# Kernel tuning notes

Measured on AMD Instinct MI355X. Metric: run time of the kernel, lower is better.

The kernel has to match this reference:

```python
import jax, jax.numpy as jnp
import numpy as np

B, S, D, H = 4, 2048, 512, 8
E = D // H  # d_head = 64

def setup_inputs() -> dict:
    key = jax.random.key(0)
    ks = jax.random.split(key, 10)
    s_in = (1.0 / np.sqrt(D))
    x  = jax.random.normal(ks[0], (B, S, D), dtype=jnp.float32)
    Wq = jax.random.normal(ks[1], (H, D, E), dtype=jnp.float32) * s_in
    bq = jax.random.normal(ks[2], (H, E), dtype=jnp.float32) * 0.01
    Wk = jax.random.normal(ks[3], (H, D, E), dtype=jnp.float32) * s_in
    bk = jax.random.normal(ks[4], (H, E), dtype=jnp.float32) * 0.01
    Wv = jax.random.normal(ks[5], (H, D, E), dtype=jnp.float32) * s_in
    bv = jax.random.normal(ks[6], (H, E), dtype=jnp.float32) * 0.01
    Wo = jax.random.normal(ks[7], (D, D), dtype=jnp.float32) * s_in
    bo = jax.random.normal(ks[8], (D,), dtype=jnp.float32) * 0.01
    return {"x": x, "Wq": Wq, "bq": bq, "Wk": Wk, "bk": bk,
            "Wv": Wv, "bv": bv, "Wo": Wo, "bo": bo}

def reference(x, Wq, bq, Wk, bk, Wv, bv, Wo, bo):
    B_, S_, D_ = x.shape
    # per-head projections (batched over head axis h)
    q = jnp.einsum('bsd,hde->bhse', x, Wq) + bq[None, :, None, :]
    k = jnp.einsum('bsd,hde->bhse', x, Wk) + bk[None, :, None, :]
    v = jnp.einsum('bsd,hde->bhse', x, Wv) + bv[None, :, None, :]
    # NOTE: original scales by d_model**-0.5 (full D), not d_head**-0.5
    scale = jnp.asarray(D_, x.dtype) ** -0.5
    scores = jnp.einsum('bhse,bhte->bhst', q, k) * scale  # [B,H,S,S]
    causal = jnp.tril(jnp.ones((S_, S_), dtype=bool))
    scores = jnp.where(causal[None, None], scores, -jnp.inf)
    attn = jax.nn.softmax(scores, axis=-1)
    out = jnp.einsum('bhst,bhte->bhse', attn, v)  # [B,H,S,E]
    # concat heads along feature dim (head-major), matching torch.cat
    out = out.transpose(0, 2, 1, 3).reshape(B_, S_, D_)
    return out @ Wo + bo  # final projection; dropout never applied in source
```

## Files before the change

### kernel.cpp

```cpp
#include <hip/hip_runtime.h>

typedef unsigned short u16;
typedef __bf16 bf16x8 __attribute__((ext_vector_type(8)));
typedef short s16x4 __attribute__((ext_vector_type(4)));
typedef short s16x8 __attribute__((ext_vector_type(8)));
typedef float f32x4 __attribute__((ext_vector_type(4)));

#define BB 4
#define SS 2048
#define DD 512
#define HH 8
#define EE 64
#define MM 8192
#define BHSE (BB*HH*SS*EE)

#define GLOBAL_AS __attribute__((address_space(1)))
#define LDS_AS    __attribute__((address_space(3)))

__device__ __forceinline__ float b2f(u16 u) {
    return __uint_as_float(((unsigned int)u) << 16);
}
__device__ __forceinline__ u16 f2b(float f) {
    unsigned int v = __float_as_uint(f);
    v += 0x7fffu + ((v >> 16) & 1u);
    return (u16)(v >> 16);
}
__device__ __forceinline__ float loadE(const void* p, size_t idx, int isbf16) {
    return isbf16 ? b2f(((const u16*)p)[idx]) : ((const float*)p)[idx];
}
__device__ __forceinline__ void load_lds16(const u16* g, u16* l) {
    __builtin_amdgcn_global_load_lds((GLOBAL_AS void*)g, (LDS_AS void*)l, 16, 0, 0);
}

__device__ __forceinline__ int detect_bf16_wave(const u16* x) {
    const int lane = threadIdx.x & 63;
    float a0 = fabsf(b2f(x[2 * lane]));
    float a1 = fabsf(b2f(x[2 * (lane + 64)]));
    int c0 = (a0 == 0.f) || (a0 > 1e-4f && a0 < 100.f);
    int c1 = (a1 == 0.f) || (a1 > 1e-4f && a1 < 100.f);
    int cnt = __popcll(__ballot(c0)) + __popcll(__ballot(c1));
    return cnt >= 96;
}

__global__ __launch_bounds__(256) void prep(
    const void* __restrict__ X,
    const void* __restrict__ Wq, const void* __restrict__ Wk,
    const void* __restrict__ Wv, const void* __restrict__ Wo,
    u16* __restrict__ Xb, u16* __restrict__ WT, u16* __restrict__ WoT,
    int* __restrict__ flag)
{
    const int isbf16 = detect_bf16_wave((const u16*)X);
    const int bid = blockIdx.x;
    const int tid = threadIdx.x;
    if (bid < 1024) {
        if (bid == 0 && tid == 0) *flag = isbf16;
        const size_t i0 = ((size_t)bid * 256 + tid) * 16;
        if (isbf16) {
            const uint4* src = (const uint4*)(((const u16*)X) + i0);
            uint4* dst = (uint4*)(Xb + i0);
            dst[0] = src[0];
            dst[1] = src[1];
        } else {
            const float* xf = ((const float*)X) + i0;
            float4 f0 = *(const float4*)xf;
            float4 f1 = *(const float4*)(xf + 4);
            float4 f2 = *(const float4*)(xf + 8);
            float4 f3 = *(const float4*)(xf + 12);
            u16 tmp[16] = { f2b(f0.x), f2b(f0.y), f2b(f0.z), f2b(f0.w),
                            f2b(f1.x), f2b(f1.y), f2b(f1.z), f2b(f1.w),
                            f2b(f2.x), f2b(f2.y), f2b(f2.z), f2b(f2.w),
                            f2b(f3.x), f2b(f3.y), f2b(f3.z), f2b(f3.w) };
            *(uint4*)(Xb + i0) = *(const uint4*)tmp;
            *(uint4*)(Xb + i0 + 8) = *(const uint4*)(tmp + 8);
        }
        return;
    }
    const int j = bid - 1024;
    const int job = j >> 6;
    const int t = j & 63;
    const void* src; u16* dst; int src_ld;
    if (job < 3) {
        const void* W = (job == 0) ? Wq : ((job == 1) ? Wk : Wv);
        int h = t >> 3, kt = t & 7;
        size_t off = (size_t)h * DD * EE + (size_t)kt * 64 * EE;
        src = isbf16 ? (const void*)(((const u16*)W) + off)
                     : (const void*)(((const float*)W) + off);
        src_ld = EE;
        dst = WT + (size_t)job * 512 * 512 + (size_t)(h * 64) * 512 + kt * 64;
    } else {
        int a = t >> 3, b = t & 7;
        size_t off = (size_t)(a * 64) * 512 + b * 64;
        src = isbf16 ? (const void*)(((const u16*)Wo) + off)
                     : (const void*)(((const float*)Wo) + off);
        src_ld = 512;
        dst = WoT + (size_t)(b * 64) * 512 + a * 64;
    }
    __shared__ __align__(16) u16 Ts[64 * 72];
#pragma unroll
    for (int it = 0; it < 2; ++it) {
        int idx = it * 256 + tid;
        int r = idx >> 3, c = (idx & 7) << 3;
        u16 tmp[8];
        if (isbf16) {
            *(bf16x8*)tmp = *(const bf16x8*)(((const u16*)src) + (size_t)r * src_ld + c);
        } else {
            const float* sp = ((const float*)src) + (size_t)r * src_ld + c;
            float4 f0 = *(const float4*)sp;
            float4 f1 = *(const float4*)(sp + 4);
            tmp[0] = f2b(f0.x); tmp[1] = f2b(f0.y); tmp[2] = f2b(f0.z); tmp[3] = f2b(f0.w);
            tmp[4] = f2b(f1.x); tmp[5] = f2b(f1.y); tmp[6] = f2b(f1.z); tmp[7] = f2b(f1.w);
        }
#pragma unroll
        for (int k = 0; k < 8; ++k) Ts[(c + k) * 72 + r] = tmp[k];
    }
    __syncthreads();
#pragma unroll
    for (int it = 0; it < 2; ++it) {
        int idx = it * 256 + tid;
        int r = idx >> 3, c = (idx & 7) << 3;
        *(bf16x8*)(dst + (size_t)r * 512 + c) = *(const bf16x8*)&Ts[r * 72 + c];
    }
}

template<int MT, int NT>
__device__ __forceinline__ void mfma_step(const u16* As, const u16* Bs,
    int mh, int nh, int lq, int quad, f32x4 acc[MT][NT])
{
    const int sw = lq & 7;
#pragma unroll
    for (int kw = 0; kw < 2; ++kw) {
        const int G = kw * 4 + quad;
        const int col = ((G ^ sw) << 3);
        bf16x8 a[MT], b[NT];
#pragma unroll
        for (int mt = 0; mt < MT; ++mt)
            a[mt] = *(const bf16x8*)&As[(mh + mt * 16 + lq) * 64 + col];
#pragma unroll
        for (int nt = 0; nt < NT; ++nt)
            b[nt] = *(const bf16x8*)&Bs[(nh + nt * 16 + lq) * 64 + col];
#pragma unroll
        for (int mt = 0; mt < MT; ++mt)
#pragma unroll
            for (int nt = 0; nt < NT; ++nt)
                acc[mt][nt] = __builtin_amdgcn_mfma_f32_16x16x32_bf16(a[mt], b[nt], acc[mt][nt], 0, 0, 0);
    }
}

__global__ __launch_bounds__(256) void gemm_qkv(
    const u16* __restrict__ Xb, const u16* __restrict__ WT,
    const void* __restrict__ bq, const void* __restrict__ bk,
    const void* __restrict__ bv, u16* __restrict__ qkv,
    const int* __restrict__ flag)
{
    const float SCALE = 0.04419417382415922f;
    const int isbf16 = *flag;
    const int l = blockIdx.x;
    const int m0 = ((l & 7) * 8 + ((l >> 3) & 7)) * 128;
    const int n0 = (l >> 6) * 128;
    const int tid = threadIdx.x;
    const int wave = tid >> 6, lane = tid & 63;
    const int lq = lane & 15, quad = lane >> 4;
    const int mh = (wave & 1) * 64, nh = (wave >> 1) * 64;
    __shared__ __align__(16) u16 As[128 * 64];
    __shared__ __align__(16) u16 Bs[128 * 64];
    f32x4 acc[4][4] = {};

    const int swz = (lane & 7) ^ ((lane >> 3) & 7);
    const size_t lane_off = (size_t)(lane >> 3) * 512 + 8 * swz;

    for (int k0 = 0; k0 < 512; k0 += 64) {
        __syncthreads();
#pragma unroll
        for (int jj = 0; jj < 4; ++jj) {
            const int c = wave * 4 + jj;
            load_lds16(Xb + (size_t)(m0 + 8 * c) * 512 + k0 + lane_off, &As[c * 512]);
            load_lds16(WT + (size_t)(n0 + 8 * c) * 512 + k0 + lane_off, &Bs[c * 512]);
        }
        __syncthreads();
        mfma_step<4, 4>(As, Bs, mh, nh, lq, quad, acc);
    }

    const int proj = n0 >> 9;
    const void* bias = (proj == 0) ? bq : ((proj == 1) ? bk : bv);
#pragma unroll
    for (int mt = 0; mt < 4; ++mt) {
#pragma unroll
        for (int nt = 0; nt < 4; ++nt) {
#pragma unroll
            for (int r = 0; r < 4; ++r) {
                int m = m0 + mh + mt * 16 + quad * 4 + r;
                int n = n0 + nh + nt * 16 + lq;
                int nn = n & 511;
                float v = acc[mt][nt][r] + loadE(bias, nn, isbf16);
                if (proj == 0) v *= SCALE;
                int b_ = m >> 11, s = m & 2047, h = nn >> 6, e = nn & 63;
                qkv[(size_t)proj * BHSE + (((size_t)(b_ * HH + h) * SS + s) * EE + e)] = f2b(v);
            }
        }
    }
}

struct Stage { uint4 k0, k1, va, vb; };

__device__ __forceinline__ void stage_load(Stage& st, const u16* Kh, const u16* Vh,
                                           int t0, int tid) {
    int r = tid >> 3, c = (tid & 7) * 8;
    st.k0 = *(const uint4*)(Kh + (size_t)(t0 + r) * 64 + c);
    st.k1 = *(const uint4*)(Kh + (size_t)(t0 + r + 32) * 64 + c);
    int t2 = 2 * (tid & 31), e8 = (tid >> 5) * 8;
    st.va = *(const uint4*)(Vh + (size_t)(t0 + t2) * 64 + e8);
    st.vb = *(const uint4*)(Vh + (size_t)(t0 + t2 + 1) * 64 + e8);
}
__device__ __forceinline__ void stage_write(const Stage& st, u16* Ksb, u16* VTsb, int tid) {
    int r = tid >> 3, c = (tid & 7) * 8;
    *(uint4*)(Ksb + r * 72 + c) = st.k0;
    *(uint4*)(Ksb + (r + 32) * 72 + c) = st.k1;
    int t2 = 2 * (tid & 31), e8 = (tid >> 5) * 8;
    int g2 = ((t2 >> 2) & 3) * 16 + ((t2 >> 4) << 2) + (t2 & 3);
    const unsigned* pa = (const unsigned*)&st.va;
    const unsigned* pb = (const unsigned*)&st.vb;
#pragma unroll
    for (int k = 0; k < 4; ++k) {
        unsigned lo = __builtin_amdgcn_perm(pb[k], pa[k], 0x05040100u);
        unsigned hi = __builtin_amdgcn_perm(pb[k], pa[k], 0x07060302u);
        *(unsigned*)(VTsb + (e8 + 2 * k) * 72 + g2) = lo;
        *(unsigned*)(VTsb + (e8 + 2 * k + 1) * 72 + g2) = hi;
    }
}

__device__ __forceinline__ void attn_tile2(const u16* Ksb, const u16* VTsb,
    const bf16x8* qf0, const bf16x8* qf1, int lq, int quad, int qh, int th,
    bool diag, f32x4 Ot[4][2], f32x4* lfrag)
{
    f32x4 sc[2][2];
#pragma unroll
    for (int tj = 0; tj < 2; ++tj) {
        const u16* Krow = Ksb + ((th * 2 + tj) * 16 + lq) * 72;
        bf16x8 k0 = *(const bf16x8*)(Krow + quad * 8);
        bf16x8 k1 = *(const bf16x8*)(Krow + 32 + quad * 8);
#pragma unroll
        for (int f = 0; f < 2; ++f) {
            f32x4 s = {};
            s = __builtin_amdgcn_mfma_f32_16x16x32_bf16(k0, qf0[f], s, 0, 0, 0);
            s = __builtin_amdgcn_mfma_f32_16x16x32_bf16(k1, qf1[f], s, 0, 0, 0);
            sc[f][tj] = s;
        }
    }
    union { unsigned u[4]; bf16x8 v; } ones;
    ones.u[0] = ones.u[1] = ones.u[2] = ones.u[3] = 0x3F803F80u;
    bf16x8 pf[2];
#pragma unroll
    for (int f = 0; f < 2; ++f) {
        unsigned pu[8];
#pragma unroll
        for (int tj = 0; tj < 2; ++tj)
#pragma unroll
            for (int r = 0; r < 4; ++r) {
                float p = __expf(sc[f][tj][r]);
                if (diag) {
                    int tl = (th * 2 + tj) * 16 + quad * 4 + r;
                    int ql = qh * 32 + f * 16 + lq;
                    p = (tl <= ql) ? p : 0.f;
                }
                pu[tj * 4 + r] = __float_as_uint(p);
            }
        union { unsigned u[4]; bf16x8 v; } w;
        w.u[0] = __builtin_amdgcn_perm(pu[1], pu[0], 0x07060302u);
        w.u[1] = __builtin_amdgcn_perm(pu[3], pu[2], 0x07060302u);
        w.u[2] = __builtin_amdgcn_perm(pu[5], pu[4], 0x07060302u);
        w.u[3] = __builtin_amdgcn_perm(pu[7], pu[6], 0x07060302u);
        pf[f] = w.v;
        lfrag[f] = __builtin_amdgcn_mfma_f32_16x16x32_bf16(ones.v, w.v, lfrag[f], 0, 0, 0);
    }
#pragma unroll
    for (int et = 0; et < 4; ++et) {
        bf16x8 vf = *(const bf16x8*)(VTsb + (et * 16 + lq) * 72 + quad * 16 + th * 8);
#pragma unroll
        for (int f = 0; f < 2; ++f)
            Ot[et][f] = __builtin_amdgcn_mfma_f32_16x16x32_bf16(vf, pf[f], Ot[et][f], 0, 0, 0);
    }
}

__global__ __launch_bounds__(256, 4) void attn_kernel(
    const u16* __restrict__ Qg, const u16* __restrict__ Kg,
    const u16* __restrict__ Vg, u16* __restrict__ Og,
    float* __restrict__ Opart, float* __restrict__ Lpart)
{
    const int bh = blockIdx.x;
    const int j  = (int)gridDim.y - 1 - (int)blockIdx.y;
    const int c  = blockIdx.z;
    if (c && j < 16) return;
    const int qb = j * 64;
    const int tFirst = c * 16;
    const int tLast  = (j < tFirst + 15) ? j : (tFirst + 15);
    const int nIt = tLast - tFirst;
    const bool diagHere = (tLast == j);
    const bool partial = (j >= 16);

    const int tid = threadIdx.x;
    const int wave = tid >> 6, lane = tid & 63;
    const int lq = lane & 15, quad = lane >> 4;
    const int qh = wave & 1, th = wave >> 1;
    const int b = bh >> 3, h = bh & 7;

    const size_t base = (size_t)bh * SS * EE;
    const u16* Kh = Kg + base;
    const u16* Vh = Vg + base;

    __shared__ __align__(16) u16 Ks[2][64 * 72];
    __shared__ __align__(16) u16 VTs[2][64 * 72];

    bf16x8 qf0[2], qf1[2];
#pragma unroll
    for (int f = 0; f < 2; ++f) {
        const int qrow_f = qb + qh * 32 + f * 16 + lq;
        const u16* Qp = Qg + base + (size_t)qrow_f * EE;
        qf0[f] = *(const bf16x8*)(Qp + quad * 8);
        qf1[f] = *(const bf16x8*)(Qp + 32 + quad * 8);
    }

    f32x4 Ot[4][2] = {};
    f32x4 lfrag[2] = {};

    Stage st;
    stage_load(st, Kh, Vh, tFirst * 64, tid);
    stage_write(st, Ks[0], VTs[0], tid);
    for (int i = 0; i <= nIt; ++i) {
        __syncthreads();
        const int cur = i & 1;
        const bool more = (i < nIt);
        if (more) stage_load(st, Kh, Vh, (tFirst + i + 1) * 64, tid);
        attn_tile2(Ks[cur], VTs[cur], qf0, qf1, lq, quad, qh, th,
                   diagHere && (i == nIt), Ot, lfrag);
        if (more) stage_write(st, Ks[cur ^ 1], VTs[cur ^ 1], tid);
    }

    __syncthreads();
    float* redO = (float*)&Ks[0][0];
    float* redL = (float*)&VTs[0][0];
    if (th == 1) {
#pragma unroll
        for (int et = 0; et < 4; ++et)
#pragma unroll
            for (int f = 0; f < 2; ++f)
                *(f32x4*)&redO[(((qh * 4 + et) * 2 + f) * 64 + lane) * 4] = Ot[et][f];
#pragma unroll
        for (int f = 0; f < 2; ++f)
            redL[(qh * 2 + f) * 64 + lane] = lfrag[f][0];
    }
    __syncthreads();
    if (th == 1) return;
    float lf[2];
#pragma unroll
    for (int f = 0; f < 2; ++f)
        lf[f] = lfrag[f][0] + redL[(qh * 2 + f) * 64 + lane];
#pragma unroll
    for (int et = 0; et < 4; ++et)
#pragma unroll
        for (int f = 0; f < 2; ++f)
            Ot[et][f] += *(const f32x4*)&redO[(((qh * 4 + et) * 2 + f) * 64 + lane) * 4];

    if (!partial) {
#pragma unroll
        for (int f = 0; f < 2; ++f) {
            const float inv = 1.f / lf[f];
            const int qrow_f = qb + qh * 32 + f * 16 + lq;
            u16* Op = Og + (((size_t)(b * SS + qrow_f)) * HH + h) * EE;
#pragma unroll
            for (int et = 0; et < 4; ++et) {
                u16 tmp[4];
#pragma unroll
                for (int r = 0; r < 4; ++r) tmp[r] = f2b(Ot[et][f][r] * inv);
                *(uint2*)(Op + et * 16 + quad * 4) = *(const uint2*)tmp;
            }
        }
    } else {
        const size_t slot = ((size_t)(bh * 16 + (j - 16)) * 2 + c);
        float* Os = Opart + slot * 4096;
#pragma unroll
        for (int f = 0; f < 2; ++f) {
            const int ql = qh * 32 + f * 16 + lq;
#pragma unroll
            for (int et = 0; et < 4; ++et)
                *(f32x4*)&Os[ql * 64 + et * 16 + quad * 4] = Ot[et][f];
            if (quad == 0) Lpart[slot * 64 + ql] = lf[f];
        }
    }
}

__global__ __launch_bounds__(256) void attn_merge(
    const float* __restrict__ Opart, const float* __restrict__ Lpart,
    u16* __restrict__ Og)
{
    const int tg = blockIdx.x * 256 + threadIdx.x;
    const int e8 = (tg & 7) * 8;
    const int rest = tg >> 3;
    const int bh = rest >> 10;
    const int sp = rest & 1023;
    const int jj = sp >> 6;
    const int ql = sp & 63;
    const size_t slot = (size_t)(bh * 16 + jj) * 2;
    const size_t o0 = slot * 4096 + (size_t)ql * 64 + e8;
    float4 a0 = *(const float4*)&Opart[o0];
    float4 a1 = *(const float4*)&Opart[o0 + 4];
    float4 b0 = *(const float4*)&Opart[o0 + 4096];
    float4 b1 = *(const float4*)&Opart[o0 + 4096 + 4];
    const size_t ls = slot * 64 + ql;
    const float inv = 1.f / (Lpart[ls] + Lpart[ls + 64]);
    const int b = bh >> 3, h = bh & 7;
    const int s = 1024 + sp;
    u16 tmp[8];
    tmp[0] = f2b((a0.x + b0.x) * inv);
    tmp[1] = f2b((a0.y + b0.y) * inv);
    tmp[2] = f2b((a0.z + b0.z) * inv);
    tmp[3] = f2b((a0.w + b0.w) * inv);
    tmp[4] = f2b((a1.x + b1.x) * inv);
    tmp[5] = f2b((a1.y + b1.y) * inv);
    tmp[6] = f2b((a1.z + b1.z) * inv);
    tmp[7] = f2b((a1.w + b1.w) * inv);
    u16* Op = Og + (((size_t)(b * SS + s)) * HH + h) * EE + e8;
    *(uint4*)Op = *(const uint4*)tmp;
}

__global__ __launch_bounds__(256) void gemm_out(
    const u16* __restrict__ A, const u16* __restrict__ WoT,
    const void* __restrict__ bo, void* __restrict__ out,
    const int* __restrict__ flag)
{
    const int isbf16 = *flag;
    const int l = blockIdx.x;
    const int m0 = ((l & 7) * 8 + ((l >> 3) & 7)) * 128;
    const int n0 = (l >> 6) * 64;
    const int tid = threadIdx.x;
    const int wave = tid >> 6, lane = tid & 63;
    const int lq = lane & 15, quad = lane >> 4;
    const int mh = (wave & 1) * 64, nh = (wave >> 1) * 32;
    __shared__ __align__(16) u16 As[128 * 64];
    __shared__ __align__(16) u16 Bs[64 * 64];
    f32x4 acc[4][2] = {};

    const int swz = (lane & 7) ^ ((lane >> 3) & 7);
    const size_t lane_off = (size_t)(lane >> 3) * 512 + 8 * swz;

    for (int k0 = 0; k0 < 512; k0 += 64) {
        __syncthreads();
#pragma unroll
        for (int jj = 0; jj < 4; ++jj) {
            const int c = wave * 4 + jj;
            load_lds16(A + (size_t)(m0 + 8 * c) * 512 + k0 + lane_off, &As[c * 512]);
        }
#pragma unroll
        for (int jj = 0; jj < 2; ++jj) {
            const int c = wave * 2 + jj;
            load_lds16(WoT + (size_t)(n0 + 8 * c) * 512 + k0 + lane_off, &Bs[c * 512]);
        }
        __syncthreads();
        mfma_step<4, 2>(As, Bs, mh, nh, lq, quad, acc);
    }
#pragma unroll
    for (int mt = 0; mt < 4; ++mt) {
#pragma unroll
        for (int nt = 0; nt < 2; ++nt) {
#pragma unroll
            for (int r = 0; r < 4; ++r) {
                int m = m0 + mh + mt * 16 + quad * 4 + r;
                int n = n0 + nh + nt * 16 + lq;
                float v = acc[mt][nt][r] + loadE(bo, n, isbf16);
                if (isbf16) ((u16*)out)[(size_t)m * 512 + n] = f2b(v);
                else        ((float*)out)[(size_t)m * 512 + n] = v;
            }
        }
    }
}

extern "C" void kernel_launch(void* const* d_in, const int* in_sizes, int n_in,
                              void* d_out, int out_size, void* d_ws, size_t ws_size,
                              hipStream_t stream) {
    const void* x  = d_in[0];
    const void* Wq = d_in[1];
    const void* bq = d_in[2];
    const void* Wk = d_in[3];
    const void* bk = d_in[4];
    const void* Wv = d_in[5];
    const void* bv = d_in[6];
    const void* Wo = d_in[7];
    const void* bo = d_in[8];

    u16* WT   = (u16*)d_ws;
    u16* WoT  = WT + 3 * 512 * 512;
    u16* qkv  = WoT + 512 * 512;
    u16* attn = qkv + 3 * (size_t)BHSE;
    int* flag = (int*)(attn + (size_t)BHSE);
    u16* Xb   = (u16*)(flag + 8);
    float* Opart = (float*)(Xb + (size_t)MM * DD);
    float* Lpart = Opart + (size_t)1024 * 4096;

    prep<<<1024 + 256, 256, 0, stream>>>(x, Wq, Wk, Wv, Wo, Xb, WT, WoT, flag);
    gemm_qkv<<<(MM / 128) * (1536 / 128), 256, 0, stream>>>(Xb, WT, bq, bk, bv, qkv, flag);
    attn_kernel<<<dim3(BB * HH, SS / 64, 2), 256, 0, stream>>>(
        qkv, qkv + BHSE, qkv + 2 * (size_t)BHSE, attn, Opart, Lpart);
    attn_merge<<<1024, 256, 0, stream>>>(Opart, Lpart, attn);
    gemm_out<<<(MM / 128) * (512 / 64), 256, 0, stream>>>(attn, WoT, bo, d_out, flag);
}
```

Measured before the change: 190.5 us.

## Stage K tiles via direct global-to-LDS loads with XOR swizzle, deeper V prefetch

K tiles now go straight from global memory into LDS through load_lds16 with an XOR-swizzled unpadded layout, instead of passing through registers. V is prefetched two tiles ahead with manual vmcnt waits and a hand-placed barrier schedule in an unrolled ping-pong loop. s_setprio is raised around the MFMA blocks. The aim is to cut register pressure and LDS write work and to overlap memory traffic with compute better. The price is fragile manual waitcnt accounting, which could be wrong if the compiler reorders memory operations.

```diff
diff --git a/kernel.cpp b/kernel.cpp
--- a/kernel.cpp
+++ b/kernel.cpp
@@ -200,21 +200,24 @@
     }
 }
 
-struct Stage { uint4 k0, k1, va, vb; };
-
-__device__ __forceinline__ void stage_load(Stage& st, const u16* Kh, const u16* Vh,
-                                           int t0, int tid) {
-    int r = tid >> 3, c = (tid & 7) * 8;
-    st.k0 = *(const uint4*)(Kh + (size_t)(t0 + r) * 64 + c);
-    st.k1 = *(const uint4*)(Kh + (size_t)(t0 + r + 32) * 64 + c);
+struct VStage { uint4 va, vb; };
+
+__device__ __forceinline__ void stageK_dma(const u16* Kh, int t0, u16* Ksb, int tid) {
+    const int wave = tid >> 6, lane = tid & 63;
+    const int r = lane >> 3, s = lane & 7;
+#pragma unroll
+    for (int jj = 0; jj < 2; ++jj) {
+        const int c = wave * 2 + jj;
+        const u16* g = Kh + (size_t)(t0 + 8 * c + r) * 64 + ((s ^ (r & 7)) << 3);
+        load_lds16(g, Ksb + c * 512);
+    }
+}
+__device__ __forceinline__ void stageV_load(VStage& st, const u16* Vh, int t0, int tid) {
     int t2 = 2 * (tid & 31), e8 = (tid >> 5) * 8;
     st.va = *(const uint4*)(Vh + (size_t)(t0 + t2) * 64 + e8);
     st.vb = *(const uint4*)(Vh + (size_t)(t0 + t2 + 1) * 64 + e8);
 }
-__device__ __forceinline__ void stage_write(const Stage& st, u16* Ksb, u16* VTsb, int tid) {
-    int r = tid >> 3, c = (tid & 7) * 8;
-    *(uint4*)(Ksb + r * 72 + c) = st.k0;
-    *(uint4*)(Ksb + (r + 32) * 72 + c) = st.k1;
+__device__ __forceinline__ void stageV_write(const VStage& st, u16* VTsb, int tid) {
     int t2 = 2 * (tid & 31), e8 = (tid >> 5) * 8;
     int g2 = ((t2 >> 2) & 3) * 16 + ((t2 >> 4) << 2) + (t2 & 3);
     const unsigned* pa = (const unsigned*)&st.va;
@@ -232,12 +235,14 @@
     const bf16x8* qf0, const bf16x8* qf1, int lq, int quad, int qh, int th,
     bool diag, f32x4 Ot[4][2], f32x4* lfrag)
 {
+    const int p0 = (quad ^ (lq & 7)) << 3;
     f32x4 sc[2][2];
 #pragma unroll
     for (int tj = 0; tj < 2; ++tj) {
-        const u16* Krow = Ksb + ((th * 2 + tj) * 16 + lq) * 72;
-        bf16x8 k0 = *(const bf16x8*)(Krow + quad * 8);
-        bf16x8 k1 = *(const bf16x8*)(Krow + 32 + quad * 8);
+        const u16* Krow = Ksb + ((th * 2 + tj) * 16 + lq) * 64;
+        bf16x8 k0 = *(const bf16x8*)(Krow + p0);
+        bf16x8 k1 = *(const bf16x8*)(Krow + (p0 ^ 32));
+        __builtin_amdgcn_s_setprio(1);
 #pragma unroll
         for (int f = 0; f < 2; ++f) {
             f32x4 s = {};
@@ -245,6 +250,7 @@
             s = __builtin_amdgcn_mfma_f32_16x16x32_bf16(k1, qf1[f], s, 0, 0, 0);
             sc[f][tj] = s;
         }
+        __builtin_amdgcn_s_setprio(0);
     }
     union { unsigned u[4]; bf16x8 v; } ones;
     ones.u[0] = ones.u[1] = ones.u[2] = ones.u[3] = 0x3F803F80u;
@@ -272,6 +278,7 @@
         pf[f] = w.v;
         lfrag[f] = __builtin_amdgcn_mfma_f32_16x16x32_bf16(ones.v, w.v, lfrag[f], 0, 0, 0);
     }
+    __builtin_amdgcn_s_setprio(1);
 #pragma unroll
     for (int et = 0; et < 4; ++et) {
         bf16x8 vf = *(const bf16x8*)(VTsb + (et * 16 + lq) * 72 + quad * 16 + th * 8);
@@ -279,7 +286,30 @@
         for (int f = 0; f < 2; ++f)
             Ot[et][f] = __builtin_amdgcn_mfma_f32_16x16x32_bf16(vf, pf[f], Ot[et][f], 0, 0, 0);
     }
-}
+    __builtin_amdgcn_s_setprio(0);
+}
+
+#define WAITV(N) asm volatile("s_waitcnt vmcnt(" #N ")" ::: "memory")
+#define SBAR0()  __builtin_amdgcn_sched_barrier(0)
+
+#define ATTN_ITER(i, CUR, STOLD, STNEW)                                        \
+  {                                                                            \
+    const bool m1 = ((i) + 1 <= nIt), m2 = ((i) + 2 <= nIt);                   \
+    if (m1) stageK_dma(Kh, (tFirst + (i) + 1) * 64, Ks[(CUR) ^ 1], tid);       \
+    SBAR0();                                                                   \
+    if (m2) stageV_load(STNEW, Vh, (tFirst + (i) + 2) * 64, tid);              \
+    SBAR0();                                                                   \
+    attn_tile2(Ks[CUR], VTs[CUR], qf0, qf1, lq, quad, qh, th,                  \
+               diagHere && ((i) == nIt), Ot, lfrag);                           \
+    if (m1) {                                                                  \
+      if (m2) { WAITV(4); } else { WAITV(2); }                                 \
+      stageV_write(STOLD, VTs[(CUR) ^ 1], tid);                                \
+      if (m2) { WAITV(2); } else { WAITV(0); }                                 \
+    }                                                                          \
+    asm volatile("s_waitcnt lgkmcnt(0)" ::: "memory");                         \
+    __builtin_amdgcn_s_barrier();                                              \
+    SBAR0();                                                                   \
+  }
 
 __global__ __launch_bounds__(256, 4) void attn_kernel(
     const u16* __restrict__ Qg, const u16* __restrict__ Kg,
@@ -307,7 +337,7 @@
     const u16* Kh = Kg + base;
     const u16* Vh = Vg + base;
 
-    __shared__ __align__(16) u16 Ks[2][64 * 72];
+    __shared__ __align__(16) u16 Ks[2][64 * 64];
     __shared__ __align__(16) u16 VTs[2][64 * 72];
 
     bf16x8 qf0[2], qf1[2];
@@ -321,18 +351,29 @@
 
     f32x4 Ot[4][2] = {};
     f32x4 lfrag[2] = {};
-
-    Stage st;
-    stage_load(st, Kh, Vh, tFirst * 64, tid);
-    stage_write(st, Ks[0], VTs[0], tid);
-    for (int i = 0; i <= nIt; ++i) {
-        __syncthreads();
-        const int cur = i & 1;
-        const bool more = (i < nIt);
-        if (more) stage_load(st, Kh, Vh, (tFirst + i + 1) * 64, tid);
-        attn_tile2(Ks[cur], VTs[cur], qf0, qf1, lq, quad, qh, th,
-                   diagHere && (i == nIt), Ot, lfrag);
-        if (more) stage_write(st, Ks[cur ^ 1], VTs[cur ^ 1], tid);
+    VStage stA, stB;
+
+    stageK_dma(Kh, tFirst * 64, Ks[0], tid);
+    SBAR0();
+    stageV_load(stA, Vh, tFirst * 64, tid);
+    SBAR0();
+    if (nIt >= 1) {
+        stageV_load(stB, Vh, (tFirst + 1) * 64, tid);
+        SBAR0();
+        WAITV(2);
+    } else {
+        WAITV(0);
+    }
+    stageV_write(stA, VTs[0], tid);
+    asm volatile("s_waitcnt lgkmcnt(0)" ::: "memory");
+    __builtin_amdgcn_s_barrier();
+    SBAR0();
+
+    for (int i = 0; ; i += 2) {
+        ATTN_ITER(i, 0, stB, stA);
+        if (i + 1 > nIt) break;
+        ATTN_ITER(i + 1, 1, stA, stB);
+        if (i + 2 > nIt) break;
     }
 
     __syncthreads();
```

Result: faster. 176.3 us (-7.5%).
